# Performance work log

Hardware: AMD Instinct MI355X
Metric: run time of the kernel (lower is better)

The kernel has to match this reference:

```python
import jax, jax.numpy as jnp
import numpy as np

TEMPERATURE = 0.5


def setup_inputs() -> dict:
    key = jax.random.key(0)
    k1, k2 = jax.random.split(key)
    B, D = 8192, 128
    z_i = jax.random.normal(k1, (B, D), dtype=jnp.float32)
    z_j = jax.random.normal(k2, (B, D), dtype=jnp.float32)
    return {"z_i": z_i, "z_j": z_j}


def reference(z_i, z_j):
    B = z_i.shape[0]
    eps = 1e-12  # matches torch F.normalize default clamp
    zi = z_i / jnp.maximum(jnp.linalg.norm(z_i, axis=1, keepdims=True), eps)
    zj = z_j / jnp.maximum(jnp.linalg.norm(z_j, axis=1, keepdims=True), eps)
    reps = jnp.concatenate([zi, zj], axis=0)  # [2B, D], unit rows
    # cosine similarity of unit vectors == dot product -> single GEMM
    sim = reps @ reps.T  # [2B, 2B]
    n = 2 * B
    diag = jnp.eye(n, dtype=bool)
    sim = jnp.where(diag, -1e9, sim) / TEMPERATURE
    labels = jnp.concatenate([jnp.arange(B) + B, jnp.arange(B)])  # positive pair indices
    logp = jax.nn.log_softmax(sim, axis=1)
    loss = -jnp.mean(jnp.take_along_axis(logp, labels[:, None], axis=1))
    return loss
```

## Files before the change

kernel.cpp:

```cpp
#include <hip/hip_runtime.h>
#include <hip/hip_bf16.h>

#define NB 8192
#define ND 128
#define N2 16384

#define CPB 1024
#define CTILE 128
#define NT (CPB / CTILE)

typedef __attribute__((ext_vector_type(4))) float f32x4;
typedef __attribute__((ext_vector_type(4))) int v4i;
typedef __attribute__((ext_vector_type(8))) int v8i;

static constexpr float SQRT_C_VAL = 1.69864368f;

__global__ __launch_bounds__(256) void nrm_kernel(const float* __restrict__ zi,
                                                  const float* __restrict__ zj,
                                                  unsigned short* __restrict__ reps8_u16,
                                                  float* __restrict__ pos,
                                                  float* __restrict__ ssum) {
    const int gtid = blockIdx.x * 256 + threadIdx.x;
    if (gtid < N2) ssum[gtid] = 0.f;
    const int pair = gtid >> 6;
    const int lane = threadIdx.x & 63;
    const float2 vi = *reinterpret_cast<const float2*>(zi + pair * ND + lane * 2);
    const float2 vj = *reinterpret_cast<const float2*>(zj + pair * ND + lane * 2);
    float ssi = vi.x * vi.x + vi.y * vi.y;
    float ssj = vj.x * vj.x + vj.y * vj.y;
#pragma unroll
    for (int m = 1; m < 64; m <<= 1) {
        ssi += __shfl_xor(ssi, m);
        ssj += __shfl_xor(ssj, m);
    }
    float ni = fmaxf(sqrtf(ssi), 1e-12f);
    float nj = fmaxf(sqrtf(ssj), 1e-12f);
    const float ii = 1.0f / ni, ij = 1.0f / nj;
    const float uix = vi.x * ii, uiy = vi.y * ii;
    const float ujx = vj.x * ij, ujy = vj.y * ij;
    float d = uix * ujx + uiy * ujy;
#pragma unroll
    for (int m = 1; m < 64; m <<= 1) d += __shfl_xor(d, m);
    if (lane == 0) pos[pair] = d;
    const int pki = __builtin_amdgcn_cvt_pk_fp8_f32(uix * SQRT_C_VAL, uiy * SQRT_C_VAL, 0, false);
    const int pkj = __builtin_amdgcn_cvt_pk_fp8_f32(ujx * SQRT_C_VAL, ujy * SQRT_C_VAL, 0, false);
    reps8_u16[pair * 64 + lane] = (unsigned short)(pki & 0xFFFF);
    reps8_u16[(NB + pair) * 64 + lane] = (unsigned short)(pkj & 0xFFFF);
}

__device__ inline void gload_lds16(const void* g, void* l) {
    __builtin_amdgcn_global_load_lds(
        (const __attribute__((address_space(1))) void*)g,
        (__attribute__((address_space(3))) void*)l, 16, 0, 0);
}

__global__ __launch_bounds__(256, 2) void sim_kernel(const char* __restrict__ reps8,
                                                     float* __restrict__ ssum) {
    __shared__ __align__(16) char lds[2][CTILE * 128];
    const int tid = threadIdx.x;
    const int lane = tid & 63;
    const int wid = tid >> 6;
    const int l15 = lane & 15;
    const int l4 = lane >> 4;
    const int rb = blockIdx.x * 256;
    const int cb = blockIdx.y * CPB;
    const int qb = rb + wid * 64;

    v8i qf[4];
#pragma unroll
    for (int g = 0; g < 4; ++g)
        qf[g] = *reinterpret_cast<const v8i*>(
            reps8 + (size_t)(qb + g * 16 + l15) * 128 + l4 * 32);

    f32x4 sacc[4];
#pragma unroll
    for (int g = 0; g < 4; ++g) sacc[g] = {0.f, 0.f, 0.f, 0.f};

    auto stage = [&](int buf, int t) {
        const int colbase = cb + t * CTILE;
#pragma unroll
        for (int it = 0; it < 4; ++it) {
            const int s_lin = it * 256 + tid;
            const int m = s_lin >> 4;
            const int sp = s_lin & 15;
            const int s = sp ^ (m & 15);
            const int col = 2 * m + (s >> 3);
            const int c = s & 7;
            const char* src = reps8 + (size_t)(colbase + col) * 128 + c * 16;
            char* dst = &lds[buf][it * 4096 + wid * 1024];
            gload_lds16(src, dst);
        }
    };

    stage(0, 0);
    __syncthreads();
    int cur = 0;
    for (int t = 0; t < NT; ++t) {
        if (t + 1 < NT) stage(cur ^ 1, t + 1);
        const int tc = cb + t * CTILE;
        const bool dg = ((unsigned)(qb - tc) < 128u);
#pragma unroll
        for (int cg = 0; cg < 8; ++cg) {
            const int col = cg * 16 + l15;
            const int m = col >> 1;
            const int slo = (((col & 1) << 3) + 2 * l4) ^ (m & 15);
            const char* lb = &lds[cur][m * 256];
            const v4i lo = *reinterpret_cast<const v4i*>(lb + slo * 16);
            const v4i hi = *reinterpret_cast<const v4i*>(lb + (slo ^ 1) * 16);
            const v8i kf = __builtin_shufflevector(lo, hi, 0, 1, 2, 3, 4, 5, 6, 7);
            const f32x4 z4 = {0.f, 0.f, 0.f, 0.f};
#pragma unroll
            for (int g = 0; g < 4; ++g) {
                f32x4 acc = __builtin_amdgcn_mfma_scale_f32_16x16x128_f8f6f4(
                    qf[g], kf, z4, 0, 0, 0, 0x7F7F7F7F, 0, 0x7F7F7F7F);
                f32x4 e;
#pragma unroll
                for (int r = 0; r < 4; ++r) e[r] = __builtin_amdgcn_exp2f(acc[r]);
                if (dg) {
                    const int col_abs = tc + col;
                    const int row0 = qb + g * 16 + l4 * 4;
#pragma unroll
                    for (int r = 0; r < 4; ++r)
                        if (row0 + r == col_abs) e[r] = 0.f;
                }
                sacc[g] += e;
            }
        }
        __syncthreads();
        cur ^= 1;
    }

#pragma unroll
    for (int g = 0; g < 4; ++g) {
#pragma unroll
        for (int r = 0; r < 4; ++r) {
#pragma unroll
            for (int m = 1; m < 16; m <<= 1) sacc[g][r] += __shfl_xor(sacc[g][r], m);
        }
    }
    if (l15 == 0) {
#pragma unroll
        for (int g = 0; g < 4; ++g)
#pragma unroll
            for (int r = 0; r < 4; ++r)
                atomicAdd(&ssum[qb + g * 16 + l4 * 4 + r], sacc[g][r]);
    }
}

__global__ __launch_bounds__(1024) void fin_kernel(const float* __restrict__ ssum,
                                                   const float* __restrict__ pos,
                                                   float* __restrict__ out) {
    const int tid = threadIdx.x;
    float acc = 0.f;
    for (int r = tid; r < N2; r += 1024) {
        const int p = (r < NB) ? r : r - NB;
        acc += logf(ssum[r]) - 2.0f * pos[p];
    }
#pragma unroll
    for (int m = 1; m < 64; m <<= 1) acc += __shfl_xor(acc, m);
    __shared__ float red[16];
    const int wid = tid >> 6, lane = tid & 63;
    if (lane == 0) red[wid] = acc;
    __syncthreads();
    if (wid == 0) {
        float v = (lane < 16) ? red[lane] : 0.f;
#pragma unroll
        for (int m = 1; m < 16; m <<= 1) v += __shfl_xor(v, m);
        if (lane == 0) out[0] = v / (float)N2;
    }
}

extern "C" void kernel_launch(void* const* d_in, const int* in_sizes, int n_in,
                              void* d_out, int out_size, void* d_ws, size_t ws_size,
                              hipStream_t stream) {
    const float* zi = (const float*)d_in[0];
    const float* zj = (const float*)d_in[1];
    float* out = (float*)d_out;
    char* ws = (char*)d_ws;

    char* reps8 = ws;
    float* pos = (float*)(ws + (size_t)N2 * ND);
    float* ssum = pos + NB;

    nrm_kernel<<<NB / 4, 256, 0, stream>>>(zi, zj, (unsigned short*)reps8, pos, ssum);
    dim3 grid(N2 / 256, N2 / CPB);
    sim_kernel<<<grid, 256, 0, stream>>>(reps8, ssum);
    fin_kernel<<<1, 1024, 0, stream>>>(ssum, pos, out);
}
```

Baseline: 64.92 us.

## Deepen sim kernel LDS pipeline to four 64-column stages with explicit waits

The column tile shrinks from 128 to 64 and the LDS becomes a four-buffer ring, keeping three async global-to-LDS loads in flight. Explicit vmcnt waits and raw s_barrier replace the single __syncthreads double buffer. The LDS swizzle and read offsets are rebuilt for the narrower tile, and the source addresses are precomputed. MFMAs are issued in a batch under raised wave priority before the exp2 work. The aim is to hide load latency and overlap matrix and transcendental work, at the cost of a workgroup barrier after every column group, which adds sync overhead.

Result: faster. 60.62 us (-6.6%).

```diff
diff --git a/kernel.cpp b/kernel.cpp
--- a/kernel.cpp
+++ b/kernel.cpp
@@ -6,8 +6,9 @@
 #define N2 16384
 
 #define CPB 1024
-#define CTILE 128
+#define CTILE 64
 #define NT (CPB / CTILE)
+#define TILEB (CTILE * 128)
 
 typedef __attribute__((ext_vector_type(4))) float f32x4;
 typedef __attribute__((ext_vector_type(4))) int v4i;
@@ -56,7 +57,7 @@
 
 __global__ __launch_bounds__(256, 2) void sim_kernel(const char* __restrict__ reps8,
                                                      float* __restrict__ ssum) {
-    __shared__ __align__(16) char lds[2][CTILE * 128];
+    __shared__ __align__(16) char lds[4][TILEB];
     const int tid = threadIdx.x;
     const int lane = tid & 63;
     const int wid = tid >> 6;
@@ -71,53 +72,81 @@
     for (int g = 0; g < 4; ++g)
         qf[g] = *reinterpret_cast<const v8i*>(
             reps8 + (size_t)(qb + g * 16 + l15) * 128 + l4 * 32);
+    __builtin_amdgcn_sched_barrier(0);
+    asm volatile("s_waitcnt vmcnt(0)" ::: "memory");
+    __builtin_amdgcn_sched_barrier(0);
 
     f32x4 sacc[4];
 #pragma unroll
     for (int g = 0; g < 4; ++g) sacc[g] = {0.f, 0.f, 0.f, 0.f};
 
-    auto stage = [&](int buf, int t) {
-        const int colbase = cb + t * CTILE;
-#pragma unroll
-        for (int it = 0; it < 4; ++it) {
-            const int s_lin = it * 256 + tid;
-            const int m = s_lin >> 4;
-            const int sp = s_lin & 15;
-            const int s = sp ^ (m & 15);
-            const int col = 2 * m + (s >> 3);
-            const int c = s & 7;
-            const char* src = reps8 + (size_t)(colbase + col) * 128 + c * 16;
-            char* dst = &lds[buf][it * 4096 + wid * 1024];
-            gload_lds16(src, dst);
+    const char* srcq[2];
+#pragma unroll
+    for (int q = 0; q < 2; ++q) {
+        const int s_lin = q * 256 + tid;
+        const int m = s_lin >> 4;
+        const int sp = s_lin & 15;
+        const int s = sp ^ ((m & 3) << 1);
+        const int col = 2 * m + (s & 1);
+        const int chunk = s >> 1;
+        srcq[q] = reps8 + (size_t)(cb + col) * 128 + chunk * 16;
+    }
+    auto stage = [&](int t) {
+        char* dst0 = &lds[t & 3][(wid * 64) * 16];
+        char* dst1 = &lds[t & 3][(256 + wid * 64) * 16];
+        gload_lds16(srcq[0] + (size_t)t * TILEB, dst0);
+        gload_lds16(srcq[1] + (size_t)t * TILEB, dst1);
+    };
+
+    const int h = l15 >> 1;
+    const int sloA = (4 * l4 + (l15 & 1)) ^ ((h & 3) << 1);
+    const int rdlo = h * 256 + sloA * 16;
+    const int rdhi = h * 256 + (sloA ^ 2) * 16;
+
+    stage(0);
+    stage(1);
+    stage(2);
+
+    for (int t = 0; t < NT; ++t) {
+        if (t + 3 < NT) {
+            stage(t + 3);
+            __builtin_amdgcn_sched_barrier(0);
+            asm volatile("s_waitcnt vmcnt(6)" ::: "memory");
+        } else if (t + 3 == NT) {
+            asm volatile("s_waitcnt vmcnt(4)" ::: "memory");
+        } else if (t + 2 == NT) {
+            asm volatile("s_waitcnt vmcnt(2)" ::: "memory");
+        } else {
+            asm volatile("s_waitcnt vmcnt(0)" ::: "memory");
         }
-    };
-
-    stage(0, 0);
-    __syncthreads();
-    int cur = 0;
-    for (int t = 0; t < NT; ++t) {
-        if (t + 1 < NT) stage(cur ^ 1, t + 1);
+        __builtin_amdgcn_s_barrier();
+        __builtin_amdgcn_sched_barrier(0);
+
         const int tc = cb + t * CTILE;
-        const bool dg = ((unsigned)(qb - tc) < 128u);
-#pragma unroll
-        for (int cg = 0; cg < 8; ++cg) {
-            const int col = cg * 16 + l15;
-            const int m = col >> 1;
-            const int slo = (((col & 1) << 3) + 2 * l4) ^ (m & 15);
-            const char* lb = &lds[cur][m * 256];
-            const v4i lo = *reinterpret_cast<const v4i*>(lb + slo * 16);
-            const v4i hi = *reinterpret_cast<const v4i*>(lb + (slo ^ 1) * 16);
+        const bool dg = ((unsigned)(qb - tc) < 64u);
+        const char* lbase = lds[t & 3];
+#pragma unroll
+        for (int cg = 0; cg < 4; ++cg) {
+            const v4i lo = *reinterpret_cast<const v4i*>(lbase + rdlo + cg * 2048);
+            const v4i hi = *reinterpret_cast<const v4i*>(lbase + rdhi + cg * 2048);
             const v8i kf = __builtin_shufflevector(lo, hi, 0, 1, 2, 3, 4, 5, 6, 7);
+            asm volatile("s_waitcnt lgkmcnt(0)" ::: "memory");
+            __builtin_amdgcn_sched_barrier(0);
+            __builtin_amdgcn_s_setprio(1);
+            f32x4 acc[4];
             const f32x4 z4 = {0.f, 0.f, 0.f, 0.f};
 #pragma unroll
+            for (int g = 0; g < 4; ++g)
+                acc[g] = __builtin_amdgcn_mfma_scale_f32_16x16x128_f8f6f4(
+                    qf[g], kf, z4, 0, 0, 0, 0x7F7F7F7F, 0, 0x7F7F7F7F);
+            __builtin_amdgcn_s_setprio(0);
+#pragma unroll
             for (int g = 0; g < 4; ++g) {
-                f32x4 acc = __builtin_amdgcn_mfma_scale_f32_16x16x128_f8f6f4(
-                    qf[g], kf, z4, 0, 0, 0, 0x7F7F7F7F, 0, 0x7F7F7F7F);
                 f32x4 e;
 #pragma unroll
-                for (int r = 0; r < 4; ++r) e[r] = __builtin_amdgcn_exp2f(acc[r]);
+                for (int r = 0; r < 4; ++r) e[r] = __builtin_amdgcn_exp2f(acc[g][r]);
                 if (dg) {
-                    const int col_abs = tc + col;
+                    const int col_abs = tc + cg * 16 + l15;
                     const int row0 = qb + g * 16 + l4 * 4;
 #pragma unroll
                     for (int r = 0; r < 4; ++r)
@@ -125,9 +154,8 @@
                 }
                 sacc[g] += e;
             }
+            __builtin_amdgcn_s_barrier();
         }
-        __syncthreads();
-        cur ^= 1;
     }
 
 #pragma unroll
```
